# Performance work log

Measured on AMD Instinct MI355X. Metric: run time of the kernel, lower is better.

## Reference

```python
import jax, jax.numpy as jnp
import numpy as np

B, N, D, H, R, K = 64, 197, 768, 3072, 16, 1


def setup_inputs() -> dict:
    key = jax.random.key(0)
    ks = jax.random.split(key, 9)
    s1 = 1.0 / np.sqrt(D)
    s2 = 1.0 / np.sqrt(H)
    return {
        "x": jax.random.normal(ks[0], (B, N, D), dtype=jnp.float32),
        "W1": jax.random.normal(ks[1], (H, D), dtype=jnp.float32) * s1,
        "b1": jax.random.normal(ks[2], (H,), dtype=jnp.float32) * s1,
        "A1": jax.random.normal(ks[3], (K, R, D), dtype=jnp.float32) * s1,
        "B1": jax.random.normal(ks[4], (K, H, R), dtype=jnp.float32) * 0.01,
        "W2": jax.random.normal(ks[5], (D, H), dtype=jnp.float32) * s2,
        "b2": jax.random.normal(ks[6], (D,), dtype=jnp.float32) * s2,
        "A2": jax.random.normal(ks[7], (K, R, H), dtype=jnp.float32) * s2,
        "B2": jax.random.normal(ks[8], (K, D, R), dtype=jnp.float32) * 0.01,
    }


def _lora(x, A, Bm):
    # result of torch: (B @ (A @ x^T.unsqueeze(1))).sum(1).transpose(1,2)
    # A: [K, r, d_in], Bm: [K, d_out, r], x: [b, n, d_in] -> [b, n, d_out]
    t = jnp.einsum('krd,bnd->bknr', A, x)          # low-rank projection
    return jnp.einsum('kor,bknr->bno', Bm, t)      # expand + sum over K


def reference(x, W1, b1, A1, B1, W2, b2, A2, B2):
    # fc1 (Linear + LoRA correction)
    h = jnp.einsum('bnd,hd->bnh', x, W1) + b1 + _lora(x, A1, B1)
    # exact (erf-based) GELU, matching torch nn.GELU default
    h = jax.nn.gelu(h, approximate=False)
    # dropout p=0 and norm=Identity by default -> no-ops
    out = jnp.einsum('bnh,dh->bnd', h, W2) + b2 + _lora(h, A2, B2)
    return out
```

## Files before the change

### kernel.cpp

```cpp
#include <hip/hip_runtime.h>
#include <math.h>

#define M_ROWS 12608
#define D_DIM  768
#define H_DIM  3072

typedef __bf16 bf16_t;
typedef __bf16 bf16x8 __attribute__((ext_vector_type(8)));
typedef float  f32x4  __attribute__((ext_vector_type(4)));

__device__ __forceinline__ float gelu_fast(float v) {
  float v2 = v * v;
  float z = v * fmaf(0.044715f, v2, 1.0f);
  float e = __expf(-1.5957691216057308f * z);
  return v * __builtin_amdgcn_rcpf(1.0f + e);
}

__global__ void cast_f32_bf16_kernel(const float* __restrict__ in,
                                     bf16_t* __restrict__ out, long n) {
  long i = ((long)blockIdx.x * 256 + threadIdx.x) * 4;
  if (i + 3 < n) {
    float4 v = *(const float4*)(in + i);
    out[i + 0] = (bf16_t)v.x; out[i + 1] = (bf16_t)v.y;
    out[i + 2] = (bf16_t)v.z; out[i + 3] = (bf16_t)v.w;
  } else {
    for (; i < n; ++i) out[i] = (bf16_t)in[i];
  }
}

__global__ void fold_lora_kernel(const float* __restrict__ W,
                                 const float* __restrict__ A,
                                 const float* __restrict__ Bm,
                                 bf16_t* __restrict__ Weff,
                                 int OUT, int IN) {
  long idx = (long)blockIdx.x * 256 + threadIdx.x;
  if (idx >= (long)OUT * IN) return;
  int o = (int)(idx / IN);
  int i = (int)(idx - (long)o * IN);
  float s = W[idx];
#pragma unroll
  for (int r = 0; r < 16; ++r)
    s += Bm[o * 16 + r] * A[r * IN + i];
  Weff[idx] = (bf16_t)s;
}

template <bool GELU, typename OutT, int SCHED, int SMEM_BYTES>
__global__ __launch_bounds__(256, 3) void gemm_kernel(
    const bf16_t* __restrict__ Amat, const bf16_t* __restrict__ Bmat,
    const float* __restrict__ bias, OutT* __restrict__ Cmat,
    int Mrows, int Ncols, int Kd) {
  __shared__ char smem[SMEM_BYTES];
  bf16_t* lds = (bf16_t*)smem;
  float* sT = (float*)smem;

  int rowb, colb;
  const int xcd = blockIdx.x & 7, t = blockIdx.x >> 3;
  if (SCHED == 1) {
    colb = t / 13;
    rowb = (t % 13) * 8 + xcd;
    if (rowb >= 99) return;
  } else {
    rowb = (t / 3) * 4 + (xcd & 3);
    if (rowb >= 99) return;
    colb = (xcd >> 2) * 3 + (t % 3);
  }
  const int row0 = rowb * 128, col0 = colb * 128;

  const int tid = threadIdx.x, lane = tid & 63, wave = tid >> 6;
  const int wm = wave & 1, wn = wave >> 1;

  const bf16_t* gA[4]; const bf16_t* gB[4];
  int offA[4], offB[4];
#pragma unroll
  for (int q = 0; q < 4; ++q) {
    int c = tid + q * 256;
    int r = c >> 3, kkg = c & 7;
    int ra = row0 + r; if (ra > Mrows - 1) ra = Mrows - 1;
    gA[q] = Amat + (size_t)ra * Kd + kkg * 8;
    offA[q] = r * 64 + (kkg ^ (r & 7)) * 8;
    gB[q] = Bmat + (size_t)(col0 + r) * Kd + kkg * 8;
    offB[q] = 8192 + r * 64 + (kkg ^ (r & 7)) * 8;
  }

  const int rl = lane & 15, kc = lane >> 4;
  int aoffs[4], boffs[4];
#pragma unroll
  for (int i = 0; i < 4; ++i) {
    int ra = wm * 64 + i * 16 + rl;
    int rb = wn * 64 + i * 16 + rl;
    aoffs[i] = ra * 64 + ((kc ^ (ra & 7)) * 8);
    boffs[i] = 8192 + rb * 64 + ((kc ^ (rb & 7)) * 8);
  }

  f32x4 acc[4][4] = {};
  f32x4 pA[4], pB[4];
  const int iters = Kd / 64;

#pragma unroll
  for (int q = 0; q < 4; ++q) {
    pA[q] = *(const f32x4*)gA[q]; pB[q] = *(const f32x4*)gB[q];
    gA[q] += 64; gB[q] += 64;
  }
#pragma unroll
  for (int q = 0; q < 4; ++q) {
    *(f32x4*)(lds + offA[q]) = pA[q];
    *(f32x4*)(lds + offB[q]) = pB[q];
  }
  __syncthreads();

  for (int it = 0; it < iters; ++it) {
    const bool more = (it + 1 < iters);
    if (more) {
#pragma unroll
      for (int q = 0; q < 4; ++q) {
        pA[q] = *(const f32x4*)gA[q]; pB[q] = *(const f32x4*)gB[q];
        gA[q] += 64; gB[q] += 64;
      }
    }
#pragma unroll
    for (int ks = 0; ks < 2; ++ks) {
      bf16x8 af[4], bfr[4];
#pragma unroll
      for (int i = 0; i < 4; ++i) af[i] = *(const bf16x8*)(lds + (aoffs[i] ^ (ks * 32)));
#pragma unroll
      for (int i = 0; i < 4; ++i) bfr[i] = *(const bf16x8*)(lds + (boffs[i] ^ (ks * 32)));
#pragma unroll
      for (int mi = 0; mi < 4; ++mi)
#pragma unroll
        for (int ni = 0; ni < 4; ++ni)
          acc[mi][ni] = __builtin_amdgcn_mfma_f32_16x16x32_bf16(
              af[mi], bfr[ni], acc[mi][ni], 0, 0, 0);
    }
    if (more) {
      __syncthreads();
#pragma unroll
      for (int q = 0; q < 4; ++q) {
        *(f32x4*)(lds + offA[q]) = pA[q];
        *(f32x4*)(lds + offB[q]) = pB[q];
      }
      __syncthreads();
    }
  }

  const int crow = (lane >> 4) * 4, ccol = lane & 15;
  if constexpr (GELU) {
    __syncthreads();
#pragma unroll
    for (int p = 0; p < 2; ++p) {
#pragma unroll
      for (int s = 0; s < 2; ++s) {
        int mi = 2 * p + s;
#pragma unroll
        for (int ni = 0; ni < 4; ++ni)
#pragma unroll
          for (int r = 0; r < 4; ++r)
            sT[(wm * 32 + s * 16 + crow + r) * 132 + wn * 64 + ni * 16 + ccol] =
                acc[mi][ni][r];
      }
      __syncthreads();
      const int erow = tid >> 2, eseg = tid & 3;
      const int grow = row0 + (erow >> 5) * 64 + (2 * p + ((erow >> 4) & 1)) * 16 + (erow & 15);
      if (grow < Mrows) {
        const float* src = sT + erow * 132 + eseg * 32;
        const float* bsrc = bias + col0 + eseg * 32;
        bf16_t ov[32];
#pragma unroll
        for (int i = 0; i < 32; ++i)
          ov[i] = (bf16_t)gelu_fast(src[i] + bsrc[i]);
        bf16_t* dst = (bf16_t*)Cmat + (size_t)grow * Ncols + col0 + eseg * 32;
#pragma unroll
        for (int k = 0; k < 4; ++k)
          *(bf16x8*)(dst + k * 8) = *(bf16x8*)(ov + k * 8);
      }
      __syncthreads();
    }
  } else {
#pragma unroll
    for (int ni = 0; ni < 4; ++ni) {
      const int gc = col0 + wn * 64 + ni * 16 + ccol;
      const float bv = bias[gc];
#pragma unroll
      for (int mi = 0; mi < 4; ++mi) {
        const int gr = row0 + wm * 64 + mi * 16 + crow;
#pragma unroll
        for (int r = 0; r < 4; ++r) {
          const int row = gr + r;
          if (row < Mrows)
            Cmat[(size_t)row * Ncols + gc] = acc[mi][ni][r] + bv;
        }
      }
    }
  }
}

extern "C" void kernel_launch(void* const* d_in, const int* in_sizes, int n_in,
                              void* d_out, int out_size, void* d_ws, size_t ws_size,
                              hipStream_t stream) {
  const float* x  = (const float*)d_in[0];
  const float* W1 = (const float*)d_in[1];
  const float* b1 = (const float*)d_in[2];
  const float* A1 = (const float*)d_in[3];
  const float* B1 = (const float*)d_in[4];
  const float* W2 = (const float*)d_in[5];
  const float* b2 = (const float*)d_in[6];
  const float* A2 = (const float*)d_in[7];
  const float* B2 = (const float*)d_in[8];
  float* out = (float*)d_out;

  char* ws = (char*)d_ws;
  bf16_t* xb    = (bf16_t*)ws;
  bf16_t* W1eff = (bf16_t*)(ws + 19366144);
  bf16_t* W2eff = (bf16_t*)(ws + 19366144 + 4718592);
  bf16_t* hbuf  = (bf16_t*)(ws + 19366144 + 2 * 4718592);

  const long nx = (long)M_ROWS * D_DIM;
  cast_f32_bf16_kernel<<<(int)((nx / 4 + 255) / 256), 256, 0, stream>>>(x, xb, nx);

  const int foldBlocks = (H_DIM * D_DIM + 255) / 256;
  fold_lora_kernel<<<foldBlocks, 256, 0, stream>>>(W1, A1, B1, W1eff, H_DIM, D_DIM);
  fold_lora_kernel<<<foldBlocks, 256, 0, stream>>>(W2, A2, B2, W2eff, D_DIM, H_DIM);

  gemm_kernel<true, bf16_t, 1, 33792><<<2496, 256, 0, stream>>>(
      xb, W1eff, b1, hbuf, M_ROWS, H_DIM, D_DIM);
  gemm_kernel<false, float, 2, 32768><<<600, 256, 0, stream>>>(
      hbuf, W2eff, b2, out, M_ROWS, D_DIM, H_DIM);
}
```

Measured before the change: 293.7 us.

## Double-buffer GEMM LDS tiles and vectorize cast and LoRA-fold kernels

The GEMM now keeps two 32KB LDS buffers and alternates between them, so each K-iteration needs one barrier instead of two. The price is 64KB of shared memory and launch bounds lowered from 3 to 2 blocks per CU. The cast kernel now handles 16 elements per thread with vector stores, and the fold kernel handles 8 contiguous outputs per thread using float4 loads, which cuts scalar memory traffic in these preprocessing kernels. The lower occupancy may offset the saving from fewer barriers.

```diff
diff --git a/kernel.cpp b/kernel.cpp
--- a/kernel.cpp
+++ b/kernel.cpp
@@ -18,11 +18,19 @@
 
 __global__ void cast_f32_bf16_kernel(const float* __restrict__ in,
                                      bf16_t* __restrict__ out, long n) {
-  long i = ((long)blockIdx.x * 256 + threadIdx.x) * 4;
-  if (i + 3 < n) {
-    float4 v = *(const float4*)(in + i);
-    out[i + 0] = (bf16_t)v.x; out[i + 1] = (bf16_t)v.y;
-    out[i + 2] = (bf16_t)v.z; out[i + 3] = (bf16_t)v.w;
+  long i = ((long)blockIdx.x * 256 + threadIdx.x) * 16;
+  if (i + 15 < n) {
+    float4 v[4];
+#pragma unroll
+    for (int q = 0; q < 4; ++q) v[q] = *(const float4*)(in + i + q * 4);
+    bf16_t ov[16];
+#pragma unroll
+    for (int q = 0; q < 4; ++q) {
+      ov[q * 4 + 0] = (bf16_t)v[q].x; ov[q * 4 + 1] = (bf16_t)v[q].y;
+      ov[q * 4 + 2] = (bf16_t)v[q].z; ov[q * 4 + 3] = (bf16_t)v[q].w;
+    }
+    *(bf16x8*)(out + i) = *(bf16x8*)ov;
+    *(bf16x8*)(out + i + 8) = *(bf16x8*)(ov + 8);
   } else {
     for (; i < n; ++i) out[i] = (bf16_t)in[i];
   }
@@ -33,23 +41,40 @@
                                  const float* __restrict__ Bm,
                                  bf16_t* __restrict__ Weff,
                                  int OUT, int IN) {
+  const int nseg = IN >> 3;
   long idx = (long)blockIdx.x * 256 + threadIdx.x;
-  if (idx >= (long)OUT * IN) return;
-  int o = (int)(idx / IN);
-  int i = (int)(idx - (long)o * IN);
-  float s = W[idx];
-#pragma unroll
-  for (int r = 0; r < 16; ++r)
-    s += Bm[o * 16 + r] * A[r * IN + i];
-  Weff[idx] = (bf16_t)s;
-}
-
-template <bool GELU, typename OutT, int SCHED, int SMEM_BYTES>
-__global__ __launch_bounds__(256, 3) void gemm_kernel(
+  if (idx >= (long)OUT * nseg) return;
+  int o = (int)(idx / nseg);
+  int s = (int)(idx - (long)o * nseg);
+  const float* wp = W + (size_t)o * IN + s * 8;
+  float4 w0 = *(const float4*)wp, w1 = *(const float4*)(wp + 4);
+  float acc[8] = {w0.x, w0.y, w0.z, w0.w, w1.x, w1.y, w1.z, w1.w};
+  float4 b4[4];
+#pragma unroll
+  for (int q = 0; q < 4; ++q) b4[q] = *(const float4*)(Bm + o * 16 + q * 4);
+  const float* bb = (const float*)b4;
+#pragma unroll
+  for (int r = 0; r < 16; ++r) {
+    float b = bb[r];
+    const float* ap = A + (size_t)r * IN + s * 8;
+    float4 a0 = *(const float4*)ap, a1 = *(const float4*)(ap + 4);
+    acc[0] = fmaf(b, a0.x, acc[0]); acc[1] = fmaf(b, a0.y, acc[1]);
+    acc[2] = fmaf(b, a0.z, acc[2]); acc[3] = fmaf(b, a0.w, acc[3]);
+    acc[4] = fmaf(b, a1.x, acc[4]); acc[5] = fmaf(b, a1.y, acc[5]);
+    acc[6] = fmaf(b, a1.z, acc[6]); acc[7] = fmaf(b, a1.w, acc[7]);
+  }
+  bf16_t ov[8];
+#pragma unroll
+  for (int i = 0; i < 8; ++i) ov[i] = (bf16_t)acc[i];
+  *(bf16x8*)(Weff + (size_t)o * IN + s * 8) = *(bf16x8*)ov;
+}
+
+template <bool GELU, typename OutT, int SCHED>
+__global__ __launch_bounds__(256, 2) void gemm_kernel(
     const bf16_t* __restrict__ Amat, const bf16_t* __restrict__ Bmat,
     const float* __restrict__ bias, OutT* __restrict__ Cmat,
     int Mrows, int Ncols, int Kd) {
-  __shared__ char smem[SMEM_BYTES];
+  __shared__ char smem[65536];
   bf16_t* lds = (bf16_t*)smem;
   float* sT = (float*)smem;
 
@@ -106,7 +131,6 @@
     *(f32x4*)(lds + offA[q]) = pA[q];
     *(f32x4*)(lds + offB[q]) = pB[q];
   }
-  __syncthreads();
 
   for (int it = 0; it < iters; ++it) {
     const bool more = (it + 1 < iters);
@@ -117,13 +141,15 @@
         gA[q] += 64; gB[q] += 64;
       }
     }
+    __syncthreads();
+    const bf16_t* buf = lds + (it & 1) * 16384;
 #pragma unroll
     for (int ks = 0; ks < 2; ++ks) {
       bf16x8 af[4], bfr[4];
 #pragma unroll
-      for (int i = 0; i < 4; ++i) af[i] = *(const bf16x8*)(lds + (aoffs[i] ^ (ks * 32)));
-#pragma unroll
-      for (int i = 0; i < 4; ++i) bfr[i] = *(const bf16x8*)(lds + (boffs[i] ^ (ks * 32)));
+      for (int i = 0; i < 4; ++i) af[i] = *(const bf16x8*)(buf + (aoffs[i] ^ (ks * 32)));
+#pragma unroll
+      for (int i = 0; i < 4; ++i) bfr[i] = *(const bf16x8*)(buf + (boffs[i] ^ (ks * 32)));
 #pragma unroll
       for (int mi = 0; mi < 4; ++mi)
 #pragma unroll
@@ -132,13 +158,12 @@
               af[mi], bfr[ni], acc[mi][ni], 0, 0, 0);
     }
     if (more) {
-      __syncthreads();
+      bf16_t* nbuf = lds + ((it + 1) & 1) * 16384;
 #pragma unroll
       for (int q = 0; q < 4; ++q) {
-        *(f32x4*)(lds + offA[q]) = pA[q];
-        *(f32x4*)(lds + offB[q]) = pB[q];
-      }
-      __syncthreads();
+        *(f32x4*)(nbuf + offA[q]) = pA[q];
+        *(f32x4*)(nbuf + offB[q]) = pB[q];
+      }
     }
   }
 
@@ -214,14 +239,13 @@
   bf16_t* hbuf  = (bf16_t*)(ws + 19366144 + 2 * 4718592);
 
   const long nx = (long)M_ROWS * D_DIM;
-  cast_f32_bf16_kernel<<<(int)((nx / 4 + 255) / 256), 256, 0, stream>>>(x, xb, nx);
-
-  const int foldBlocks = (H_DIM * D_DIM + 255) / 256;
-  fold_lora_kernel<<<foldBlocks, 256, 0, stream>>>(W1, A1, B1, W1eff, H_DIM, D_DIM);
-  fold_lora_kernel<<<foldBlocks, 256, 0, stream>>>(W2, A2, B2, W2eff, D_DIM, H_DIM);
-
-  gemm_kernel<true, bf16_t, 1, 33792><<<2496, 256, 0, stream>>>(
+  cast_f32_bf16_kernel<<<(int)(nx / 16 / 256 + 1), 256, 0, stream>>>(x, xb, nx);
+
+  fold_lora_kernel<<<1152, 256, 0, stream>>>(W1, A1, B1, W1eff, H_DIM, D_DIM);
+  fold_lora_kernel<<<1152, 256, 0, stream>>>(W2, A2, B2, W2eff, D_DIM, H_DIM);
+
+  gemm_kernel<true, bf16_t, 1><<<2496, 256, 0, stream>>>(
       xb, W1eff, b1, hbuf, M_ROWS, H_DIM, D_DIM);
-  gemm_kernel<false, float, 2, 32768><<<600, 256, 0, stream>>>(
+  gemm_kernel<false, float, 2><<<600, 256, 0, stream>>>(
       hbuf, W2eff, b2, out, M_ROWS, D_DIM, H_DIM);
 }
```

Result: slower. 319.9 us (+8.9%).
